# Optimization experiments

Measured on AMD Instinct MI355X. Metric: run time of the kernel, lower is better.

The kernel has to match this reference:

```python
import jax, jax.numpy as jnp
import numpy as np

B, S, D = 8, 4096, 64
LN_EPS = 1e-3  # keras LayerNormalization default epsilon


def setup_inputs() -> dict:
    key = jax.random.key(0)
    k1, k2 = jax.random.split(key)
    x = jax.random.normal(k1, (B, S, D), dtype=jnp.float32)
    # (D,D,D) concept tensor, scaled small like glorot-ish init
    concept_map = jax.random.normal(k2, (D, D, D), dtype=jnp.float32) * 0.02
    gamma = jnp.ones((D,), dtype=jnp.float32)
    beta = jnp.zeros((D,), dtype=jnp.float32)
    return {"x": x, "concept_map": concept_map, "gamma": gamma, "beta": beta}


def reference(x, concept_map, gamma, beta):
    b, s, d = x.shape
    # Causal Toeplitz decay matrix: T[i, j] = 1/(i-j)^2 for j < i, else 0.
    idx = jnp.arange(s)
    diff = idx[:, None] - idx[None, :]  # (S, S)
    T = jnp.where(diff > 0, 1.0 / (jnp.maximum(diff, 1).astype(x.dtype) ** 2), 0.0)
    # Weighted causal prefix sum: S_pre[b, i, c] = sum_{j<i} x[b, j, c] / (i-j)^2
    s_pre = jnp.einsum('ij,bjc->bic', T, x)
    # Bilinear form with concept tensor: out[b,i,k] = sum_{a,c} x[b,i,a] * s_pre[b,i,c] * W[k,a,c]
    outer = (x[:, :, :, None] * s_pre[:, :, None, :]).reshape(b, s, d * d)  # (B,S,D*D)
    out = outer @ concept_map.reshape(d, d * d).T  # (B,S,D)
    # Residual + LayerNorm (axis=-1, keras defaults). Dropout is identity at inference.
    r = out + x
    mu = jnp.mean(r, axis=-1, keepdims=True)
    var = jnp.mean((r - mu) ** 2, axis=-1, keepdims=True)
    y = (r - mu) / jnp.sqrt(var + LN_EPS) * gamma + beta
    return y
```

## Files before the change

### kernel.cpp

```cpp
#include <hip/hip_runtime.h>

#define S_DIM 4096
#define B_DIM 8
#define D_DIM 64
#define LN_EPS 1e-3f

typedef _Float16 half8 __attribute__((ext_vector_type(8)));
typedef float f32x4 __attribute__((ext_vector_type(4)));

__device__ __forceinline__ void async_copy16(void* lds, const void* gsrc) {
    __builtin_amdgcn_global_load_lds(
        (const __attribute__((address_space(1))) unsigned int*)gsrc,
        (__attribute__((address_space(3))) unsigned int*)lds, 16, 0, 0);
}

__global__ __launch_bounds__(256) void prep_stage1(const float* __restrict__ x,
                                                   const float* __restrict__ W,
                                                   _Float16* __restrict__ wt,
                                                   _Float16* __restrict__ s_out) {
    if (blockIdx.x < 1024) {
        int idx = blockIdx.x * 256 + threadIdx.x;
        int a = idx >> 12;
        int k = (idx >> 6) & 63;
        int c = idx & 63;
        wt[idx] = (_Float16)W[((k << 6) + a) * 64 + c];
        return;
    }
    const int lin = blockIdx.x - 1024;
    const int it = lin & 63;
    const int by = lin >> 6;
    const int i0 = it * 64;
    const int tid = threadIdx.x;
    const int w = tid >> 6, l = tid & 63, lg = l >> 4, lr = l & 15;

    __shared__ _Float16 Bs[64 * 72];

    f32x4 acc[4] = {};
    const float iRowF = (float)(i0 + w * 16 + lr);
    const int ldC = tid & 63;
    const int ldJ = (tid >> 6) * 16;

    const int jt0 = (it >= 2) ? (it - 2) : 0;
    for (int jt = jt0; jt <= it; ++jt) {
        const int j0 = jt * 64;
        __syncthreads();
        {
            const float* xp = x + ((size_t)by * S_DIM + j0 + ldJ) * D_DIM + ldC;
            half8 v0, v1;
            #pragma unroll
            for (int q = 0; q < 8; ++q) {
                v0[q] = (_Float16)xp[q * D_DIM];
                v1[q] = (_Float16)xp[(8 + q) * D_DIM];
            }
            *(half8*)&Bs[ldC * 72 + ldJ] = v0;
            *(half8*)&Bs[ldC * 72 + ldJ + 8] = v1;
        }
        __syncthreads();
        #pragma unroll
        for (int kk = 0; kk < 2; ++kk) {
            half8 af;
            #pragma unroll
            for (int bq = 0; bq < 8; ++bq) {
                int j = j0 + kk * 32 + lg * 8 + bq;
                float df = iRowF - (float)j;
                float tv = (df > 0.f) ? __builtin_amdgcn_rcpf(df * df) : 0.f;
                af[bq] = (_Float16)tv;
            }
            #pragma unroll
            for (int nt = 0; nt < 4; ++nt) {
                half8 bf = *(const half8*)&Bs[(nt * 16 + lr) * 72 + kk * 32 + lg * 8];
                acc[nt] = __builtin_amdgcn_mfma_f32_16x16x32_f16(af, bf, acc[nt], 0, 0, 0);
            }
        }
    }

    #pragma unroll
    for (int nt = 0; nt < 4; ++nt) {
        #pragma unroll
        for (int r = 0; r < 4; ++r) {
            int i = i0 + w * 16 + lg * 4 + r;
            int c = nt * 16 + lr;
            s_out[((size_t)by * S_DIM + i) * D_DIM + c] = (_Float16)acc[nt][r];
        }
    }
}

__global__ __launch_bounds__(256, 2) void stage2(const float* __restrict__ x,
                                                 const _Float16* __restrict__ s,
                                                 const _Float16* __restrict__ wt,
                                                 const float* __restrict__ gamma,
                                                 const float* __restrict__ beta,
                                                 float* __restrict__ out) {
    const int r0 = blockIdx.x * 64;
    const int tid = threadIdx.x;
    const int w = tid >> 6, l = tid & 63, lg = l >> 4, lr = l & 15;

    __shared__ __align__(16) char smem[65536];
    char* myBuf = smem + w * 16384;

    const int laneSrc = ((l >> 3) * 128) + ((((l & 7) ^ (l >> 3)) << 4));
    const char* wbase = (const char*)wt + (size_t)w * 16 * 8192;

#define STAGEW(t_, buf_)                                                       \
    {                                                                          \
        _Pragma("unroll")                                                      \
        for (int s_ = 0; s_ < 8; ++s_)                                         \
            async_copy16(myBuf + (buf_) * 8192 + s_ * 1024,                    \
                         wbase + (size_t)(t_) * 8192 + s_ * 1024 + laneSrc);   \
    }

    half8 sf[4][2];
    #pragma unroll
    for (int rt = 0; rt < 4; ++rt) {
        size_t row = (size_t)(r0 + rt * 16 + lr) * 64;
        sf[rt][0] = *(const half8*)&s[row + lg * 8];
        sf[rt][1] = *(const half8*)&s[row + 32 + lg * 8];
    }
    half8 xav[4][2];
    #pragma unroll
    for (int rt = 0; rt < 4; ++rt) {
        const float* xp = x + (size_t)(r0 + rt * 16 + lr) * 64 + w * 16;
        half8 h0, h1;
        #pragma unroll
        for (int j = 0; j < 8; ++j) {
            h0[j] = (_Float16)xp[j];
            h1[j] = (_Float16)xp[8 + j];
        }
        xav[rt][0] = h0;
        xav[rt][1] = h1;
    }

    __builtin_amdgcn_sched_barrier(0);
    STAGEW(0, 0);
    STAGEW(1, 1);
    __builtin_amdgcn_sched_barrier(0);
    asm volatile("s_waitcnt vmcnt(0)" ::: "memory");
    __builtin_amdgcn_sched_barrier(0);

    f32x4 acc[4][4] = {};
    const int swz0 = (lg * 16) ^ ((lr & 7) << 4);
    const int swz1 = (64 + lg * 16) ^ ((lr & 7) << 4);

    #pragma unroll
    for (int t = 0; t < 16; ++t) {
        const char* wa = myBuf + (t & 1) * 8192;
        half8 af[4][2];
        #pragma unroll
        for (int rt = 0; rt < 4; ++rt) {
            _Float16 xa = xav[rt][t >> 3][t & 7];
            af[rt][0] = sf[rt][0] * xa;
            af[rt][1] = sf[rt][1] * xa;
        }
        #pragma unroll
        for (int nt = 0; nt < 4; ++nt) {
            const char* rp = wa + (nt * 16 + lr) * 128;
            half8 b0 = *(const half8*)(rp + swz0);
            half8 b1 = *(const half8*)(rp + swz1);
            #pragma unroll
            for (int rt = 0; rt < 4; ++rt) {
                acc[rt][nt] = __builtin_amdgcn_mfma_f32_16x16x32_f16(af[rt][0], b0, acc[rt][nt], 0, 0, 0);
                acc[rt][nt] = __builtin_amdgcn_mfma_f32_16x16x32_f16(af[rt][1], b1, acc[rt][nt], 0, 0, 0);
            }
        }
        if (t + 2 < 16) {
            __builtin_amdgcn_sched_barrier(0);
            STAGEW(t + 2, t & 1);
            asm volatile("s_waitcnt vmcnt(8)" ::: "memory");
            __builtin_amdgcn_sched_barrier(0);
        } else if (t == 14) {
            asm volatile("s_waitcnt vmcnt(0)" ::: "memory");
            __builtin_amdgcn_sched_barrier(0);
        }
    }

    float* Pw = (float*)myBuf;
    #pragma unroll
    for (int rt = 0; rt < 4; ++rt)
        #pragma unroll
        for (int nt = 0; nt < 4; ++nt)
            #pragma unroll
            for (int reg = 0; reg < 4; ++reg)
                Pw[(rt * 16 + lg * 4 + reg) * 64 + nt * 16 + lr] = acc[rt][nt][reg];
    __syncthreads();

    const float* P0 = (const float*)(smem);
    const float* P1 = (const float*)(smem + 16384);
    const float* P2 = (const float*)(smem + 32768);
    const float* P3 = (const float*)(smem + 49152);

    float gba[4], bta[4];
    #pragma unroll
    for (int nt = 0; nt < 4; ++nt) {
        gba[nt] = gamma[nt * 16 + lr];
        bta[nt] = beta[nt * 16 + lr];
    }

    float rv[4][4], sum[4], ssq[4];
    #pragma unroll
    for (int reg = 0; reg < 4; ++reg) {
        const int row_l = w * 16 + lg * 4 + reg;
        const float* xr = x + (size_t)(r0 + row_l) * 64;
        float s_ = 0.f, q_ = 0.f;
        #pragma unroll
        for (int nt = 0; nt < 4; ++nt) {
            const int col = nt * 16 + lr;
            const int o = row_l * 64 + col;
            float v = P0[o] + P1[o] + P2[o] + P3[o] + xr[col];
            rv[nt][reg] = v;
            s_ += v;
            q_ += v * v;
        }
        sum[reg] = s_;
        ssq[reg] = q_;
    }
    #pragma unroll
    for (int m = 1; m < 16; m <<= 1) {
        #pragma unroll
        for (int reg = 0; reg < 4; ++reg) {
            sum[reg] += __shfl_xor(sum[reg], m, 64);
            ssq[reg] += __shfl_xor(ssq[reg], m, 64);
        }
    }
    #pragma unroll
    for (int reg = 0; reg < 4; ++reg) {
        float mean = sum[reg] * (1.f / 64.f);
        float var = ssq[reg] * (1.f / 64.f) - mean * mean;
        float rstd = __frsqrt_rn(var + LN_EPS);
        const int gr = r0 + w * 16 + lg * 4 + reg;
        #pragma unroll
        for (int nt = 0; nt < 4; ++nt) {
            float y = (rv[nt][reg] - mean) * rstd * gba[nt] + bta[nt];
            out[(size_t)gr * 64 + nt * 16 + lr] = y;
        }
    }
#undef STAGEW
}

extern "C" void kernel_launch(void* const* d_in, const int* in_sizes, int n_in,
                              void* d_out, int out_size, void* d_ws, size_t ws_size,
                              hipStream_t stream) {
    const float* x     = (const float*)d_in[0];
    const float* W     = (const float*)d_in[1];
    const float* gamma = (const float*)d_in[2];
    const float* beta  = (const float*)d_in[3];
    float* outp        = (float*)d_out;

    char* ws = (char*)d_ws;
    _Float16* s_f16 = (_Float16*)ws;
    _Float16* wt    = (_Float16*)(ws + (size_t)B_DIM * S_DIM * D_DIM * 2);

    prep_stage1<<<1024 + 512, 256, 0, stream>>>(x, W, wt, s_f16);
    stage2<<<(B_DIM * S_DIM) / 64, 256, 0, stream>>>(x, s_f16, wt, gamma, beta, outp);
}
```

Baseline: 33.49 us.

## Split stage2 reduction over eight waves with fp16 partial-sum reduction

Stage2 now runs 512 threads (8 waves) per 64-row block, and each wave handles 8 of the 64 'a' slices instead of 16, with half-sized async weight staging. The s tile is shared through LDS instead of being held per-wave in registers, and x is loaded with float4 vectors. Partial sums from waves 1-7 are written to LDS as fp16 and reduced by wave 0, which also does the LayerNorm. The prep kernel reorders its blocks so the stage1 blocks launch first. The goal is more waves in flight to hide latency, at the cost of more reduction traffic, a serial epilogue on one wave, and extra fp16 rounding of the partial sums.

```diff
diff --git a/kernel.cpp b/kernel.cpp
--- a/kernel.cpp
+++ b/kernel.cpp
@@ -2,10 +2,10 @@
 
 #define S_DIM 4096
 #define B_DIM 8
-#define D_DIM 64
 #define LN_EPS 1e-3f
 
 typedef _Float16 half8 __attribute__((ext_vector_type(8)));
+typedef _Float16 half2v __attribute__((ext_vector_type(2)));
 typedef float f32x4 __attribute__((ext_vector_type(4)));
 
 __device__ __forceinline__ void async_copy16(void* lds, const void* gsrc) {
@@ -18,15 +18,15 @@
                                                    const float* __restrict__ W,
                                                    _Float16* __restrict__ wt,
                                                    _Float16* __restrict__ s_out) {
-    if (blockIdx.x < 1024) {
-        int idx = blockIdx.x * 256 + threadIdx.x;
+    if (blockIdx.x >= 512) {
+        int idx = (blockIdx.x - 512) * 256 + threadIdx.x;
         int a = idx >> 12;
         int k = (idx >> 6) & 63;
         int c = idx & 63;
         wt[idx] = (_Float16)W[((k << 6) + a) * 64 + c];
         return;
     }
-    const int lin = blockIdx.x - 1024;
+    const int lin = blockIdx.x;
     const int it = lin & 63;
     const int by = lin >> 6;
     const int i0 = it * 64;
@@ -45,12 +45,12 @@
         const int j0 = jt * 64;
         __syncthreads();
         {
-            const float* xp = x + ((size_t)by * S_DIM + j0 + ldJ) * D_DIM + ldC;
+            const float* xp = x + ((size_t)by * S_DIM + j0 + ldJ) * 64 + ldC;
             half8 v0, v1;
             #pragma unroll
             for (int q = 0; q < 8; ++q) {
-                v0[q] = (_Float16)xp[q * D_DIM];
-                v1[q] = (_Float16)xp[(8 + q) * D_DIM];
+                v0[q] = (_Float16)xp[q * 64];
+                v1[q] = (_Float16)xp[(8 + q) * 64];
             }
             *(half8*)&Bs[ldC * 72 + ldJ] = v0;
             *(half8*)&Bs[ldC * 72 + ldJ + 8] = v1;
@@ -80,12 +80,12 @@
         for (int r = 0; r < 4; ++r) {
             int i = i0 + w * 16 + lg * 4 + r;
             int c = nt * 16 + lr;
-            s_out[((size_t)by * S_DIM + i) * D_DIM + c] = (_Float16)acc[nt][r];
-        }
-    }
-}
-
-__global__ __launch_bounds__(256, 2) void stage2(const float* __restrict__ x,
+            s_out[((size_t)by * S_DIM + i) * 64 + c] = (_Float16)acc[nt][r];
+        }
+    }
+}
+
+__global__ __launch_bounds__(512, 4) void stage2(const float* __restrict__ x,
                                                  const _Float16* __restrict__ s,
                                                  const _Float16* __restrict__ wt,
                                                  const float* __restrict__ gamma,
@@ -95,145 +95,167 @@
     const int tid = threadIdx.x;
     const int w = tid >> 6, l = tid & 63, lg = l >> 4, lr = l & 15;
 
-    __shared__ __align__(16) char smem[65536];
-    char* myBuf = smem + w * 16384;
+    __shared__ __align__(16) char smem[65536 + 9216];
+    char* myBuf = smem + w * 8192;
+    _Float16* sS = (_Float16*)(smem + 65536);
+    half2v* Pf = (half2v*)smem;
 
     const int laneSrc = ((l >> 3) * 128) + ((((l & 7) ^ (l >> 3)) << 4));
-    const char* wbase = (const char*)wt + (size_t)w * 16 * 8192;
-
-#define STAGEW(t_, buf_)                                                       \
+    const char* wbase = (const char*)wt + (size_t)w * 8 * 8192;
+
+#define STAGEH(hs_, buf_)                                                      \
     {                                                                          \
         _Pragma("unroll")                                                      \
-        for (int s_ = 0; s_ < 8; ++s_)                                         \
-            async_copy16(myBuf + (buf_) * 8192 + s_ * 1024,                    \
-                         wbase + (size_t)(t_) * 8192 + s_ * 1024 + laneSrc);   \
-    }
-
-    half8 sf[4][2];
+        for (int b_ = 0; b_ < 4; ++b_)                                         \
+            async_copy16(myBuf + (buf_) * 4096 + b_ * 1024,                    \
+                         wbase + (size_t)(hs_) * 4096 + b_ * 1024 + laneSrc);  \
+    }
+
+    STAGEH(0, 0);
+    STAGEH(1, 1);
+
+    {
+        int row = tid >> 3, c0 = (tid & 7) * 8;
+        half8 sv = *(const half8*)&s[(size_t)(r0 + row) * 64 + c0];
+        *(half8*)&sS[row * 72 + c0] = sv;
+    }
+
+    half8 xav[4];
     #pragma unroll
     for (int rt = 0; rt < 4; ++rt) {
-        size_t row = (size_t)(r0 + rt * 16 + lr) * 64;
-        sf[rt][0] = *(const half8*)&s[row + lg * 8];
-        sf[rt][1] = *(const half8*)&s[row + 32 + lg * 8];
-    }
-    half8 xav[4][2];
-    #pragma unroll
-    for (int rt = 0; rt < 4; ++rt) {
-        const float* xp = x + (size_t)(r0 + rt * 16 + lr) * 64 + w * 16;
-        half8 h0, h1;
-        #pragma unroll
-        for (int j = 0; j < 8; ++j) {
-            h0[j] = (_Float16)xp[j];
-            h1[j] = (_Float16)xp[8 + j];
-        }
-        xav[rt][0] = h0;
-        xav[rt][1] = h1;
-    }
-
-    __builtin_amdgcn_sched_barrier(0);
-    STAGEW(0, 0);
-    STAGEW(1, 1);
-    __builtin_amdgcn_sched_barrier(0);
-    asm volatile("s_waitcnt vmcnt(0)" ::: "memory");
-    __builtin_amdgcn_sched_barrier(0);
+        const float* xp = x + (size_t)(r0 + rt * 16 + lr) * 64 + w * 8;
+        float4 v0 = *(const float4*)xp;
+        float4 v1 = *(const float4*)(xp + 4);
+        half8 h;
+        h[0] = (_Float16)v0.x; h[1] = (_Float16)v0.y;
+        h[2] = (_Float16)v0.z; h[3] = (_Float16)v0.w;
+        h[4] = (_Float16)v1.x; h[5] = (_Float16)v1.y;
+        h[6] = (_Float16)v1.z; h[7] = (_Float16)v1.w;
+        xav[rt] = h;
+    }
+
+    __syncthreads();
 
     f32x4 acc[4][4] = {};
     const int swz0 = (lg * 16) ^ ((lr & 7) << 4);
     const int swz1 = (64 + lg * 16) ^ ((lr & 7) << 4);
 
     #pragma unroll
-    for (int t = 0; t < 16; ++t) {
-        const char* wa = myBuf + (t & 1) * 8192;
-        half8 af[4][2];
+    for (int hs = 0; hs < 16; ++hs) {
+        const int h = hs & 1;
+        const char* wa = myBuf + h * 4096;
+        const char* rp0 = wa + lr * 128;
+        const char* rp1 = wa + (16 + lr) * 128;
+        half8 b00 = *(const half8*)(rp0 + swz0);
+        half8 b01 = *(const half8*)(rp0 + swz1);
+        half8 b10 = *(const half8*)(rp1 + swz0);
+        half8 b11 = *(const half8*)(rp1 + swz1);
+
+        __builtin_amdgcn_s_setprio(1);
         #pragma unroll
         for (int rt = 0; rt < 4; ++rt) {
-            _Float16 xa = xav[rt][t >> 3][t & 7];
-            af[rt][0] = sf[rt][0] * xa;
-            af[rt][1] = sf[rt][1] * xa;
-        }
-        #pragma unroll
-        for (int nt = 0; nt < 4; ++nt) {
-            const char* rp = wa + (nt * 16 + lr) * 128;
-            half8 b0 = *(const half8*)(rp + swz0);
-            half8 b1 = *(const half8*)(rp + swz1);
-            #pragma unroll
-            for (int rt = 0; rt < 4; ++rt) {
-                acc[rt][nt] = __builtin_amdgcn_mfma_f32_16x16x32_f16(af[rt][0], b0, acc[rt][nt], 0, 0, 0);
-                acc[rt][nt] = __builtin_amdgcn_mfma_f32_16x16x32_f16(af[rt][1], b1, acc[rt][nt], 0, 0, 0);
-            }
-        }
-        if (t + 2 < 16) {
+            _Float16 xa = xav[rt][hs >> 1];
+            half8 s0 = *(const half8*)&sS[(rt * 16 + lr) * 72 + lg * 8];
+            half8 s1 = *(const half8*)&sS[(rt * 16 + lr) * 72 + 32 + lg * 8];
+            half8 a0 = s0 * xa;
+            half8 a1 = s1 * xa;
+            acc[rt][h * 2 + 0] = __builtin_amdgcn_mfma_f32_16x16x32_f16(a0, b00, acc[rt][h * 2 + 0], 0, 0, 0);
+            acc[rt][h * 2 + 0] = __builtin_amdgcn_mfma_f32_16x16x32_f16(a1, b01, acc[rt][h * 2 + 0], 0, 0, 0);
+            acc[rt][h * 2 + 1] = __builtin_amdgcn_mfma_f32_16x16x32_f16(a0, b10, acc[rt][h * 2 + 1], 0, 0, 0);
+            acc[rt][h * 2 + 1] = __builtin_amdgcn_mfma_f32_16x16x32_f16(a1, b11, acc[rt][h * 2 + 1], 0, 0, 0);
+        }
+        __builtin_amdgcn_s_setprio(0);
+
+        if (hs < 14) {
             __builtin_amdgcn_sched_barrier(0);
-            STAGEW(t + 2, t & 1);
-            asm volatile("s_waitcnt vmcnt(8)" ::: "memory");
+            STAGEH(hs + 2, h);
+            asm volatile("s_waitcnt vmcnt(4)" ::: "memory");
             __builtin_amdgcn_sched_barrier(0);
-        } else if (t == 14) {
+        } else if (hs == 14) {
             asm volatile("s_waitcnt vmcnt(0)" ::: "memory");
             __builtin_amdgcn_sched_barrier(0);
         }
     }
-
-    float* Pw = (float*)myBuf;
-    #pragma unroll
-    for (int rt = 0; rt < 4; ++rt)
-        #pragma unroll
-        for (int nt = 0; nt < 4; ++nt)
-            #pragma unroll
-            for (int reg = 0; reg < 4; ++reg)
-                Pw[(rt * 16 + lg * 4 + reg) * 64 + nt * 16 + lr] = acc[rt][nt][reg];
+#undef STAGEH
+
     __syncthreads();
-
-    const float* P0 = (const float*)(smem);
-    const float* P1 = (const float*)(smem + 16384);
-    const float* P2 = (const float*)(smem + 32768);
-    const float* P3 = (const float*)(smem + 49152);
-
-    float gba[4], bta[4];
-    #pragma unroll
-    for (int nt = 0; nt < 4; ++nt) {
-        gba[nt] = gamma[nt * 16 + lr];
-        bta[nt] = beta[nt * 16 + lr];
-    }
-
-    float rv[4][4], sum[4], ssq[4];
-    #pragma unroll
-    for (int reg = 0; reg < 4; ++reg) {
-        const int row_l = w * 16 + lg * 4 + reg;
-        const float* xr = x + (size_t)(r0 + row_l) * 64;
-        float s_ = 0.f, q_ = 0.f;
+    if (w != 0) {
+        const int ph = w - 1;
+        #pragma unroll
+        for (int rt = 0; rt < 4; ++rt)
+            #pragma unroll
+            for (int nt = 0; nt < 4; ++nt) {
+                int base = (((ph * 4 + rt) * 4 + nt) * 2) * 64 + l;
+                half2v p01 = { (_Float16)acc[rt][nt][0], (_Float16)acc[rt][nt][1] };
+                half2v p23 = { (_Float16)acc[rt][nt][2], (_Float16)acc[rt][nt][3] };
+                Pf[base] = p01;
+                Pf[base + 64] = p23;
+            }
+    }
+    __syncthreads();
+
+    if (w == 0) {
+        float gba[4], bta[4];
         #pragma unroll
         for (int nt = 0; nt < 4; ++nt) {
-            const int col = nt * 16 + lr;
-            const int o = row_l * 64 + col;
-            float v = P0[o] + P1[o] + P2[o] + P3[o] + xr[col];
-            rv[nt][reg] = v;
-            s_ += v;
-            q_ += v * v;
-        }
-        sum[reg] = s_;
-        ssq[reg] = q_;
-    }
-    #pragma unroll
-    for (int m = 1; m < 16; m <<= 1) {
-        #pragma unroll
-        for (int reg = 0; reg < 4; ++reg) {
-            sum[reg] += __shfl_xor(sum[reg], m, 64);
-            ssq[reg] += __shfl_xor(ssq[reg], m, 64);
-        }
-    }
-    #pragma unroll
-    for (int reg = 0; reg < 4; ++reg) {
-        float mean = sum[reg] * (1.f / 64.f);
-        float var = ssq[reg] * (1.f / 64.f) - mean * mean;
-        float rstd = __frsqrt_rn(var + LN_EPS);
-        const int gr = r0 + w * 16 + lg * 4 + reg;
-        #pragma unroll
-        for (int nt = 0; nt < 4; ++nt) {
-            float y = (rv[nt][reg] - mean) * rstd * gba[nt] + bta[nt];
-            out[(size_t)gr * 64 + nt * 16 + lr] = y;
-        }
-    }
-#undef STAGEW
+            gba[nt] = gamma[nt * 16 + lr];
+            bta[nt] = beta[nt * 16 + lr];
+        }
+        #pragma unroll
+        for (int rt = 0; rt < 4; ++rt) {
+            float rv[4][4], sum[4], ssq[4];
+            #pragma unroll
+            for (int nt = 0; nt < 4; ++nt) {
+                float v0 = acc[rt][nt][0], v1 = acc[rt][nt][1];
+                float v2 = acc[rt][nt][2], v3 = acc[rt][nt][3];
+                #pragma unroll
+                for (int ph = 0; ph < 7; ++ph) {
+                    int base = (((ph * 4 + rt) * 4 + nt) * 2) * 64 + l;
+                    half2v q01 = Pf[base];
+                    half2v q23 = Pf[base + 64];
+                    v0 += (float)q01[0]; v1 += (float)q01[1];
+                    v2 += (float)q23[0]; v3 += (float)q23[1];
+                }
+                acc[rt][nt][0] = v0; acc[rt][nt][1] = v1;
+                acc[rt][nt][2] = v2; acc[rt][nt][3] = v3;
+            }
+            #pragma unroll
+            for (int reg = 0; reg < 4; ++reg) {
+                const int row_l = rt * 16 + lg * 4 + reg;
+                const float* xr = x + (size_t)(r0 + row_l) * 64;
+                float s_ = 0.f, q_ = 0.f;
+                #pragma unroll
+                for (int nt = 0; nt < 4; ++nt) {
+                    float v = acc[rt][nt][reg] + xr[nt * 16 + lr];
+                    rv[nt][reg] = v;
+                    s_ += v;
+                    q_ += v * v;
+                }
+                sum[reg] = s_;
+                ssq[reg] = q_;
+            }
+            #pragma unroll
+            for (int m = 1; m < 16; m <<= 1) {
+                #pragma unroll
+                for (int reg = 0; reg < 4; ++reg) {
+                    sum[reg] += __shfl_xor(sum[reg], m, 64);
+                    ssq[reg] += __shfl_xor(ssq[reg], m, 64);
+                }
+            }
+            #pragma unroll
+            for (int reg = 0; reg < 4; ++reg) {
+                float mean = sum[reg] * (1.f / 64.f);
+                float var = ssq[reg] * (1.f / 64.f) - mean * mean;
+                float rstd = __frsqrt_rn(var + LN_EPS);
+                const int gr = r0 + rt * 16 + lg * 4 + reg;
+                #pragma unroll
+                for (int nt = 0; nt < 4; ++nt) {
+                    float y = (rv[nt][reg] - mean) * rstd * gba[nt] + bta[nt];
+                    out[(size_t)gr * 64 + nt * 16 + lr] = y;
+                }
+            }
+        }
+    }
 }
 
 extern "C" void kernel_launch(void* const* d_in, const int* in_sizes, int n_in,
@@ -247,8 +269,8 @@
 
     char* ws = (char*)d_ws;
     _Float16* s_f16 = (_Float16*)ws;
-    _Float16* wt    = (_Float16*)(ws + (size_t)B_DIM * S_DIM * D_DIM * 2);
-
-    prep_stage1<<<1024 + 512, 256, 0, stream>>>(x, W, wt, s_f16);
-    stage2<<<(B_DIM * S_DIM) / 64, 256, 0, stream>>>(x, s_f16, wt, gamma, beta, outp);
-}
+    _Float16* wt    = (_Float16*)(ws + (size_t)B_DIM * S_DIM * 64 * 2);
+
+    prep_stage1<<<1536, 256, 0, stream>>>(x, W, wt, s_f16);
+    stage2<<<(B_DIM * S_DIM) / 64, 512, 0, stream>>>(x, s_f16, wt, gamma, beta, outp);
+}
```

Result: slower. 44.43 us (+32.6%).
